# Kernel optimization log

Measured on AMD Instinct MI355X. Metric: run time of the kernel, lower is better.

The kernel has to match this reference:

```python
import jax, jax.numpy as jnp
import numpy as np

N_EMBED = 1024
N_HEADS = 16
HEAD_DIM = N_EMBED // N_HEADS


def setup_inputs() -> dict:
    key = jax.random.key(0)
    ks = jax.random.split(key, 5)
    x = jax.random.normal(ks[0], (4, 2048, N_EMBED), dtype=jnp.float32)
    # Linear params stored as [in, out] (y = x @ W + b), math-equivalent to torch Linear
    scale_attn = 1.0 / np.sqrt(N_EMBED)
    W_attn = jax.random.normal(ks[1], (N_EMBED, 3 * N_EMBED), dtype=jnp.float32) * scale_attn
    b_attn = jax.random.normal(ks[2], (3 * N_EMBED,), dtype=jnp.float32) * 0.02
    W_proj = jax.random.normal(ks[3], (N_EMBED, N_EMBED), dtype=jnp.float32) * scale_attn
    b_proj = jax.random.normal(ks[4], (N_EMBED,), dtype=jnp.float32) * 0.02
    return {"x": x, "W_attn": W_attn, "b_attn": b_attn, "W_proj": W_proj, "b_proj": b_proj}


def reference(x, W_attn, b_attn, W_proj, b_proj):
    BS, SL, ED = x.shape
    qkv = x @ W_attn + b_attn                      # [B, S, 3E]
    q, k, v = jnp.split(qkv, 3, axis=2)
    # [B, H, S, D]
    def heads(t):
        return t.reshape(BS, SL, N_HEADS, HEAD_DIM).transpose(0, 2, 1, 3)
    q, k, v = heads(q), heads(k), heads(v)
    att = jnp.einsum('bhqd,bhkd->bhqk', q, k) * (HEAD_DIM ** -0.5)
    causal = jnp.tril(jnp.ones((SL, SL), dtype=bool))
    att = jnp.where(causal[None, None], att, -jnp.inf)
    att = jax.nn.softmax(att, axis=-1)
    y = jnp.einsum('bhqk,bhkd->bhqd', att, v)      # [B, H, S, D]
    y = y.transpose(0, 2, 1, 3).reshape(BS, SL, ED)
    return y @ W_proj + b_proj
```

## Files before the change

kernel.cpp:

```cpp
#include <hip/hip_runtime.h>


#define BATCH 4
#define SEQ   2048
#define EMB   1024
#define NH    16
#define HD    64

typedef __bf16 bf16;
typedef __bf16 bf16x8 __attribute__((ext_vector_type(8)));
typedef float  f32x4  __attribute__((ext_vector_type(4)));

__device__ __forceinline__ void ld_lds16(const void* g, void* l) {
  __builtin_amdgcn_global_load_lds(
      (const __attribute__((address_space(1))) void*)g,
      (__attribute__((address_space(3))) void*)l, 16, 0, 0);
}

__global__ void cvt_f32_bf16(const float* __restrict__ in, bf16* __restrict__ out, int n) {
  int i = (blockIdx.x * blockDim.x + threadIdx.x) * 4;
  if (i + 3 < n) {
    float4 v = *(const float4*)(in + i);
    bf16 o0 = (bf16)v.x, o1 = (bf16)v.y, o2 = (bf16)v.z, o3 = (bf16)v.w;
    out[i] = o0; out[i+1] = o1; out[i+2] = o2; out[i+3] = o3;
  }
}

__global__ void transpose_cvt2(const float* __restrict__ Wa, const float* __restrict__ Wp,
                               bf16* __restrict__ WaT, bf16* __restrict__ WpT) {
  __shared__ float tile[32][33];
  int bx = blockIdx.x;
  const float* W; bf16* WT; int N;
  if (bx < 96) { W = Wa; WT = WaT; N = 3072; }
  else         { W = Wp; WT = WpT; N = 1024; bx -= 96; }
  int n0 = bx * 32, k0 = blockIdx.y * 32;
  int tx = threadIdx.x & 31, ty = threadIdx.x >> 5;
#pragma unroll
  for (int r = 0; r < 4; r++) {
    int k = k0 + ty + r * 8;
    tile[ty + r * 8][tx] = W[(long)k * N + n0 + tx];
  }
  __syncthreads();
#pragma unroll
  for (int r = 0; r < 4; r++) {
    int n = n0 + ty + r * 8;
    WT[(long)n * EMB + k0 + tx] = (bf16)tile[tx][ty + r * 8];
  }
}

#define QSCALE 0.18033688f

__global__ __launch_bounds__(256, 2) void gemm8p(
    const bf16* __restrict__ A, const bf16* __restrict__ Bt,
    const float* __restrict__ bias,
    bf16* __restrict__ q, bf16* __restrict__ k, bf16* __restrict__ v)
{
  __shared__ __align__(16) bf16 lds[24576];
  int lin = blockIdx.x;
  int xcd = lin & 7, s = lin >> 3;
  int by = xcd * 8 + (s & 7);
  int bx = s >> 3;
  int m0 = by * 128, n0 = bx * 256;
  int t = threadIdx.x;
  int wid = t >> 6, lane = t & 63;
  int l15 = lane & 15, quad = lane >> 4;
  int wc = wid;

  const bf16* Ag = A + (long)m0 * EMB;
  const bf16* Bg = Bt + (long)n0 * EMB;

  f32x4 acc[8][4] = {};
  bf16x8 af[8], bfr[4];
  constexpr int NT = EMB / 32;
  int ph8 = ((quad + (l15 >> 1)) & 3) * 8;

#define LDSA(b) (lds + (b) * 4096)
#define LDSB(b) (lds + 8192 + (b) * 8192)

#define ISSUE64(gbase, rowoff, ldst, ktt)                                      \
  { int r_ = (rowoff) + (t >> 2);                                              \
    int g_ = ((t & 3) - ((t >> 3) & 3)) & 3;                                   \
    ld_lds16(&(gbase)[(long)r_ * EMB + (ktt) + g_ * 8],                        \
             (ldst) + ((rowoff) + wid * 16) * 32); }

#define RD_A(mi) { int r_ = (mi) * 16 + l15;                                   \
    af[mi] = *(const bf16x8*)&Ab[r_ * 32 + ph8]; }
#define RD_B(ni) { int r_ = wc * 64 + (ni) * 16 + l15;                         \
    bfr[ni] = *(const bf16x8*)&Bb[r_ * 32 + ph8]; }

#define FENCE asm volatile("" ::: "memory")
#define BAR   { FENCE; __builtin_amdgcn_s_barrier(); FENCE; }

#define MFMAC(nlo)                                                             \
  { __builtin_amdgcn_s_setprio(1);                                             \
    _Pragma("unroll") for (int mi_ = 0; mi_ < 8; ++mi_)                        \
      _Pragma("unroll") for (int nj_ = 0; nj_ < 2; ++nj_)                      \
        acc[mi_][(nlo) + nj_] = __builtin_amdgcn_mfma_f32_16x16x32_bf16(       \
            af[mi_], bfr[(nlo) + nj_], acc[mi_][(nlo) + nj_], 0, 0, 0);        \
    __builtin_amdgcn_s_setprio(0); }

  ISSUE64(Ag, 0,   LDSA(0), 0);
  ISSUE64(Ag, 64,  LDSA(0), 0);
  ISSUE64(Bg, 0,   LDSB(0), 0);
  ISSUE64(Bg, 64,  LDSB(0), 0);
  ISSUE64(Bg, 128, LDSB(0), 0);
  ISSUE64(Bg, 192, LDSB(0), 0);
  ISSUE64(Ag, 0,   LDSA(1), 32);
  asm volatile("s_waitcnt vmcnt(1)" ::: "memory");
  BAR;

#pragma unroll 2
  for (int tt = 0; tt < NT; ++tt) {
    const bf16* Ab = LDSA(tt & 1);
    const bf16* Bb = LDSB(tt & 1);
    bf16* An = LDSA((tt + 1) & 1);
    bf16* Bn = LDSB((tt + 1) & 1);
    bf16* Ac = LDSA(tt & 1);
    int kn  = (tt + 1 < NT ? tt + 1 : NT - 1) * 32;
    int kn2 = (tt + 2 < NT ? tt + 2 : NT - 1) * 32;

#pragma unroll
    for (int mi = 0; mi < 8; ++mi) RD_A(mi);
    RD_B(0); RD_B(1);
    ISSUE64(Ag, 64,  An, kn);
    ISSUE64(Bg, 0,   Bn, kn);
    ISSUE64(Bg, 64,  Bn, kn);
    ISSUE64(Bg, 128, Bn, kn);
    BAR; MFMAC(0); BAR;
    RD_B(2); RD_B(3);
    ISSUE64(Bg, 192, Bn, kn);
    ISSUE64(Ag, 0,   Ac, kn2);
    asm volatile("s_waitcnt vmcnt(1)" ::: "memory");
    BAR; MFMAC(2); BAR;
  }

  asm volatile("s_waitcnt vmcnt(0)" ::: "memory");
  __syncthreads();

  int which = bx >> 2;
  if (which < 2) {
    bf16* dst = (which == 0) ? q : k;
    float scale = (which == 0) ? QSCALE : 1.0f;
#pragma unroll
    for (int mi = 0; mi < 8; ++mi)
#pragma unroll
      for (int ni = 0; ni < 4; ++ni) {
        int gcol = n0 + wc * 64 + ni * 16 + l15;
        float bv = bias[gcol];
        int e = gcol & 1023, h = e >> 6, d = e & 63;
#pragma unroll
        for (int i = 0; i < 4; ++i) {
          int grow = m0 + mi * 16 + quad * 4 + i;
          int b = grow >> 11, ss = grow & 2047;
          dst[(((long)b * NH + h) * SEQ + ss) * HD + d] =
              (bf16)((acc[mi][ni][i] + bv) * scale);
        }
      }
  } else {
#pragma unroll
    for (int mi = 0; mi < 8; ++mi)
#pragma unroll
      for (int ni = 0; ni < 4; ++ni) {
        int gcol = n0 + wc * 64 + ni * 16 + l15;
        float bv = bias[gcol];
        int e = gcol & 1023, h = e >> 6, d = e & 63;
#pragma unroll
        for (int i = 0; i < 4; ++i) {
          int grow = m0 + mi * 16 + quad * 4 + i;
          int b = grow >> 11, ss = grow & 2047;
          v[(((long)b * NH + h) * HD + d) * SEQ + ss] =
              (bf16)(acc[mi][ni][i] + bv);
        }
      }
  }
#undef LDSA
#undef LDSB
#undef ISSUE64
#undef RD_A
#undef RD_B
#undef MFMAC
}

__global__ __launch_bounds__(256, 3) void gemm_proj(
    const bf16* __restrict__ A, const bf16* __restrict__ Bt,
    const float* __restrict__ bias, float* __restrict__ out)
{
  __shared__ __align__(16) bf16 Al[128 * 64];
  __shared__ __align__(16) bf16 Bl[64 * 64];
  int lin = blockIdx.x;
  int xcd = lin & 7, s = lin >> 3;
  int bx = s >> 3, by = xcd * 8 + (s & 7);
  int m0 = by * 128;
  int n0 = bx * 64;
  int t = threadIdx.x;
  int wave = t >> 6, lane = t & 63;
  int l15 = lane & 15, quad = lane >> 4;
  int wm = (wave & 1) * 64, wn = (wave >> 1) * 32;

  f32x4 acc[4][2] = {};

  for (int kt = 0; kt < EMB; kt += 64) {
    __syncthreads();
#pragma unroll
    for (int it = 0; it < 4; ++it) {
      int c = it * 256 + t;
      int row = c >> 3, u = c & 7;
      ld_lds16(&A[(long)(m0 + row) * EMB + kt + ((u ^ (row & 7)) * 8)],
               &Al[(it * 256 + wave * 64) * 8]);
    }
    {
      int c = t;
      int row = c >> 3, u = c & 7;
      ld_lds16(&Bt[(long)(n0 + row) * EMB + kt + ((u ^ (row & 7)) * 8)],
               &Bl[(wave * 64) * 8]);
      c = 256 + t;
      row = c >> 3; u = c & 7;
      ld_lds16(&Bt[(long)(n0 + row) * EMB + kt + ((u ^ (row & 7)) * 8)],
               &Bl[(256 + wave * 64) * 8]);
    }
    __syncthreads();
#pragma unroll
    for (int ks = 0; ks < 2; ++ks) {
      bf16x8 af[4], bfr[2];
#pragma unroll
      for (int i = 0; i < 4; ++i) {
        int r = wm + i * 16 + l15;
        af[i] = *(const bf16x8*)(&Al[r * 64 + (((ks * 4 + quad) ^ (r & 7)) * 8)]);
      }
#pragma unroll
      for (int i = 0; i < 2; ++i) {
        int r = wn + i * 16 + l15;
        bfr[i] = *(const bf16x8*)(&Bl[r * 64 + (((ks * 4 + quad) ^ (r & 7)) * 8)]);
      }
#pragma unroll
      for (int mi = 0; mi < 4; ++mi)
#pragma unroll
        for (int ni = 0; ni < 2; ++ni)
          acc[mi][ni] = __builtin_amdgcn_mfma_f32_16x16x32_bf16(af[mi], bfr[ni], acc[mi][ni], 0, 0, 0);
    }
  }

#pragma unroll
  for (int mi = 0; mi < 4; ++mi)
#pragma unroll
    for (int ni = 0; ni < 2; ++ni) {
      int gcol = n0 + wn + ni * 16 + l15;
      float bv = bias[gcol];
#pragma unroll
      for (int i = 0; i < 4; ++i) {
        int grow = m0 + wm + mi * 16 + quad * 4 + i;
        out[(long)grow * EMB + gcol] = acc[mi][ni][i] + bv;
      }
    }
}

#define LDP 72

__global__ __launch_bounds__(256, 4) void attn(
    const bf16* __restrict__ Q, const bf16* __restrict__ K,
    const bf16* __restrict__ Vt, bf16* __restrict__ Y)
{
  __shared__ __align__(16) bf16 Kl[64 * 64];
  __shared__ __align__(16) bf16 Vl[64 * 64];
  __shared__ __align__(16) bf16 Pl[4][16 * LDP];
  int L = blockIdx.x;
  int a = L >> 3;
  int hd = (L & 7) + 8 * (a & 7);
  int pr = a >> 3;
  int b = hd >> 4, h = hd & 15;
  const bf16* Qp  = Q  + (((long)b * NH + h) * SEQ) * HD;
  const bf16* Kp  = K  + (((long)b * NH + h) * SEQ) * HD;
  const bf16* Vtp = Vt + (((long)b * NH + h) * HD) * SEQ;
  int t = threadIdx.x, wave = t >> 6, lane = t & 63;
  int l15 = lane & 15, quad = lane >> 4;

#pragma unroll 1
  for (int pass = 0; pass < 2; ++pass) {
    int sp = (pass == 0) ? (31 - pr) : pr;
    int q0 = sp * 64;
    int wq0 = q0 + wave * 16;

    bf16x8 qf[2];
    {
      const bf16* qrow = Qp + (long)(wq0 + l15) * HD + quad * 8;
      qf[0] = *(const bf16x8*)(qrow);
      qf[1] = *(const bf16x8*)(qrow + 32);
    }
    float lrow[4] = {};
    f32x4 oacc[4] = {};

    int ntiles = sp + 1;
#pragma unroll 1
    for (int kt = 0; kt < ntiles; ++kt) {
      int k0 = kt * 64;
      __syncthreads();
#pragma unroll
      for (int it = 0; it < 2; ++it) {
        int cu = it * 256 + t;
        int row = cu >> 3, u = cu & 7;
        ld_lds16(&Kp[(long)(k0 + row) * HD + ((u ^ (row & 7)) * 8)],
                 &Kl[(it * 256 + wave * 64) * 8]);
        ld_lds16(&Vtp[(long)row * SEQ + k0 + ((u ^ (row & 7)) * 8)],
                 &Vl[(it * 256 + wave * 64) * 8]);
      }
      __syncthreads();

      f32x4 sc[4] = {};
#pragma unroll
      for (int kk = 0; kk < 2; ++kk) {
#pragma unroll
        for (int ni = 0; ni < 4; ++ni) {
          int r = ni * 16 + l15, u = kk * 4 + quad;
          bf16x8 kfr = *(const bf16x8*)(&Kl[r * 64 + ((u ^ (r & 7)) * 8)]);
          sc[ni] = __builtin_amdgcn_mfma_f32_16x16x32_bf16(qf[kk], kfr, sc[ni], 0, 0, 0);
        }
      }

      bool full = (k0 + 63 <= wq0);
#pragma unroll
      for (int i = 0; i < 4; ++i) {
        int qr = wq0 + quad * 4 + i;
        float e[4];
#pragma unroll
        for (int ni = 0; ni < 4; ++ni) {
          float x = sc[ni][i];
          if (!full) x = (k0 + ni * 16 + l15 <= qr) ? x : -1e30f;
          e[ni] = __builtin_amdgcn_exp2f(x);
        }
        lrow[i] += (e[0] + e[1]) + (e[2] + e[3]);
        int prow = (quad * 4 + i) * LDP;
#pragma unroll
        for (int ni = 0; ni < 4; ++ni)
          Pl[wave][prow + ni * 16 + l15] = (bf16)e[ni];
      }
      asm volatile("s_waitcnt lgkmcnt(0)" ::: "memory");
#pragma unroll
      for (int kk = 0; kk < 2; ++kk) {
        int kbase = kk * 32 + quad * 8;
        bf16x8 pf = *(const bf16x8*)(&Pl[wave][(l15) * LDP + kbase]);
#pragma unroll
        for (int ni = 0; ni < 4; ++ni) {
          int dd = ni * 16 + l15, u = kk * 4 + quad;
          bf16x8 vf = *(const bf16x8*)(&Vl[dd * 64 + ((u ^ (dd & 7)) * 8)]);
          oacc[ni] = __builtin_amdgcn_mfma_f32_16x16x32_bf16(pf, vf, oacc[ni], 0, 0, 0);
        }
      }
    }
#pragma unroll
    for (int i = 0; i < 4; ++i) {
      float rs = lrow[i];
#pragma unroll
      for (int off = 8; off; off >>= 1) rs += __shfl_xor(rs, off, 16);
      float inv = 1.0f / rs;
      int qr = wq0 + quad * 4 + i;
      bf16* dst = Y + ((long)(b * SEQ + qr)) * EMB + h * HD;
#pragma unroll
      for (int ni = 0; ni < 4; ++ni)
        dst[ni * 16 + l15] = (bf16)(oacc[ni][i] * inv);
    }
  }
}

extern "C" void kernel_launch(void* const* d_in, const int* in_sizes, int n_in,
                              void* d_out, int out_size, void* d_ws, size_t ws_size,
                              hipStream_t stream) {
  const float* x      = (const float*)d_in[0];
  const float* W_attn = (const float*)d_in[1];
  const float* b_attn = (const float*)d_in[2];
  const float* W_proj = (const float*)d_in[3];
  const float* b_proj = (const float*)d_in[4];
  float* out = (float*)d_out;
  char* ws = (char*)d_ws;
  bf16* xb  = (bf16*)(ws);
  bf16* WaT = (bf16*)(ws + 16777216);
  bf16* WpT = (bf16*)(ws + 23068672);
  bf16* Qb  = (bf16*)(ws + 25165824);
  bf16* Kb  = (bf16*)(ws + 41943040);
  bf16* Vtb = (bf16*)(ws + 58720256);
  bf16* Yb  = (bf16*)(ws + 75497472);

  cvt_f32_bf16<<<8192, 256, 0, stream>>>(x, xb, BATCH * SEQ * EMB);
  transpose_cvt2<<<dim3(128, 32), 256, 0, stream>>>(W_attn, W_proj, WaT, WpT);
  gemm8p<<<768, 256, 0, stream>>>(xb, WaT, b_attn, Qb, Kb, Vtb);
  attn<<<1024, 256, 0, stream>>>(Qb, Kb, Vtb, Yb);
  gemm_proj<<<1024, 256, 0, stream>>>(Yb, WpT, b_proj, out);
}
```

Measured before the change: 248.2 us.

## Widen QKV GEMM tiles to 128x384 with 8 waves per block

The QKV projection GEMM now uses 512-thread blocks (8 waves), each computing a 128x384 output tile with 48 columns per wave, and launches 512 blocks instead of 768. Each k-step loads the A tile with a single 128-row issue, and the B tile grows to 384 rows in a larger LDS buffer. The aim is more reuse of each A tile per block and a grid that fits the CU count in one wave. The XCD-aware block swizzle is dropped for a plain row-major order, and the epilogue now decides Q/K/V per column because a tile can cross the Q/K/V boundaries. This may hurt L2 locality across XCDs and raises per-block LDS use.

After: 262.3 us. 5.7% more time.

```diff
diff --git a/kernel.cpp b/kernel.cpp
--- a/kernel.cpp
+++ b/kernel.cpp
@@ -50,17 +50,16 @@
 
 #define QSCALE 0.18033688f
 
-__global__ __launch_bounds__(256, 2) void gemm8p(
+__global__ __launch_bounds__(512, 2) void gemm_qkv(
     const bf16* __restrict__ A, const bf16* __restrict__ Bt,
     const float* __restrict__ bias,
     bf16* __restrict__ q, bf16* __restrict__ k, bf16* __restrict__ v)
 {
-  __shared__ __align__(16) bf16 lds[24576];
+  __shared__ __align__(16) bf16 lds[32768];
   int lin = blockIdx.x;
-  int xcd = lin & 7, s = lin >> 3;
-  int by = xcd * 8 + (s & 7);
-  int bx = s >> 3;
-  int m0 = by * 128, n0 = bx * 256;
+  int bx = lin & 7;
+  int by = lin >> 3;
+  int m0 = by * 128, n0 = bx * 384;
   int t = threadIdx.x;
   int wid = t >> 6, lane = t & 63;
   int l15 = lane & 15, quad = lane >> 4;
@@ -69,15 +68,15 @@
   const bf16* Ag = A + (long)m0 * EMB;
   const bf16* Bg = Bt + (long)n0 * EMB;
 
-  f32x4 acc[8][4] = {};
-  bf16x8 af[8], bfr[4];
+  f32x4 acc[8][3] = {};
+  bf16x8 af[8], bfr[3];
   constexpr int NT = EMB / 32;
   int ph8 = ((quad + (l15 >> 1)) & 3) * 8;
 
 #define LDSA(b) (lds + (b) * 4096)
-#define LDSB(b) (lds + 8192 + (b) * 8192)
-
-#define ISSUE64(gbase, rowoff, ldst, ktt)                                      \
+#define LDSB(b) (lds + 8192 + (b) * 12288)
+
+#define ISSUE128(gbase, rowoff, ldst, ktt)                                     \
   { int r_ = (rowoff) + (t >> 2);                                              \
     int g_ = ((t & 3) - ((t >> 3) & 3)) & 3;                                   \
     ld_lds16(&(gbase)[(long)r_ * EMB + (ktt) + g_ * 8],                        \
@@ -85,27 +84,34 @@
 
 #define RD_A(mi) { int r_ = (mi) * 16 + l15;                                   \
     af[mi] = *(const bf16x8*)&Ab[r_ * 32 + ph8]; }
-#define RD_B(ni) { int r_ = wc * 64 + (ni) * 16 + l15;                         \
+#define RD_B(ni) { int r_ = wc * 48 + (ni) * 16 + l15;                         \
     bfr[ni] = *(const bf16x8*)&Bb[r_ * 32 + ph8]; }
 
 #define FENCE asm volatile("" ::: "memory")
 #define BAR   { FENCE; __builtin_amdgcn_s_barrier(); FENCE; }
 
-#define MFMAC(nlo)                                                             \
+#define MFMAC2(n0_, n1_)                                                       \
+  { __builtin_amdgcn_s_setprio(1);                                             \
+    _Pragma("unroll") for (int mi_ = 0; mi_ < 8; ++mi_) {                      \
+      acc[mi_][n0_] = __builtin_amdgcn_mfma_f32_16x16x32_bf16(                 \
+          af[mi_], bfr[n0_], acc[mi_][n0_], 0, 0, 0);                          \
+      acc[mi_][n1_] = __builtin_amdgcn_mfma_f32_16x16x32_bf16(                 \
+          af[mi_], bfr[n1_], acc[mi_][n1_], 0, 0, 0);                          \
+    }                                                                          \
+    __builtin_amdgcn_s_setprio(0); }
+
+#define MFMAC1(n0_)                                                            \
   { __builtin_amdgcn_s_setprio(1);                                             \
     _Pragma("unroll") for (int mi_ = 0; mi_ < 8; ++mi_)                        \
-      _Pragma("unroll") for (int nj_ = 0; nj_ < 2; ++nj_)                      \
-        acc[mi_][(nlo) + nj_] = __builtin_amdgcn_mfma_f32_16x16x32_bf16(       \
-            af[mi_], bfr[(nlo) + nj_], acc[mi_][(nlo) + nj_], 0, 0, 0);        \
+      acc[mi_][n0_] = __builtin_amdgcn_mfma_f32_16x16x32_bf16(                 \
+          af[mi_], bfr[n0_], acc[mi_][n0_], 0, 0, 0);                          \
     __builtin_amdgcn_s_setprio(0); }
 
-  ISSUE64(Ag, 0,   LDSA(0), 0);
-  ISSUE64(Ag, 64,  LDSA(0), 0);
-  ISSUE64(Bg, 0,   LDSB(0), 0);
-  ISSUE64(Bg, 64,  LDSB(0), 0);
-  ISSUE64(Bg, 128, LDSB(0), 0);
-  ISSUE64(Bg, 192, LDSB(0), 0);
-  ISSUE64(Ag, 0,   LDSA(1), 32);
+  ISSUE128(Ag, 0,   LDSA(0), 0);
+  ISSUE128(Bg, 0,   LDSB(0), 0);
+  ISSUE128(Bg, 128, LDSB(0), 0);
+  ISSUE128(Bg, 256, LDSB(0), 0);
+  ISSUE128(Ag, 0,   LDSA(1), 32);
   asm volatile("s_waitcnt vmcnt(1)" ::: "memory");
   BAR;
 
@@ -113,7 +119,6 @@
   for (int tt = 0; tt < NT; ++tt) {
     const bf16* Ab = LDSA(tt & 1);
     const bf16* Bb = LDSB(tt & 1);
-    bf16* An = LDSA((tt + 1) & 1);
     bf16* Bn = LDSB((tt + 1) & 1);
     bf16* Ac = LDSA(tt & 1);
     int kn  = (tt + 1 < NT ? tt + 1 : NT - 1) * 32;
@@ -122,32 +127,30 @@
 #pragma unroll
     for (int mi = 0; mi < 8; ++mi) RD_A(mi);
     RD_B(0); RD_B(1);
-    ISSUE64(Ag, 64,  An, kn);
-    ISSUE64(Bg, 0,   Bn, kn);
-    ISSUE64(Bg, 64,  Bn, kn);
-    ISSUE64(Bg, 128, Bn, kn);
-    BAR; MFMAC(0); BAR;
-    RD_B(2); RD_B(3);
-    ISSUE64(Bg, 192, Bn, kn);
-    ISSUE64(Ag, 0,   Ac, kn2);
+    ISSUE128(Bg, 0,   Bn, kn);
+    ISSUE128(Bg, 128, Bn, kn);
+    BAR; MFMAC2(0, 1); BAR;
+    RD_B(2);
+    ISSUE128(Bg, 256, Bn, kn);
+    ISSUE128(Ag, 0,   Ac, kn2);
     asm volatile("s_waitcnt vmcnt(1)" ::: "memory");
-    BAR; MFMAC(2); BAR;
+    BAR; MFMAC1(2); BAR;
   }
 
   asm volatile("s_waitcnt vmcnt(0)" ::: "memory");
   __syncthreads();
 
-  int which = bx >> 2;
-  if (which < 2) {
-    bf16* dst = (which == 0) ? q : k;
-    float scale = (which == 0) ? QSCALE : 1.0f;
-#pragma unroll
-    for (int mi = 0; mi < 8; ++mi)
-#pragma unroll
-      for (int ni = 0; ni < 4; ++ni) {
-        int gcol = n0 + wc * 64 + ni * 16 + l15;
-        float bv = bias[gcol];
-        int e = gcol & 1023, h = e >> 6, d = e & 63;
+#pragma unroll
+  for (int mi = 0; mi < 8; ++mi)
+#pragma unroll
+    for (int ni = 0; ni < 3; ++ni) {
+      int gcol = n0 + wc * 48 + ni * 16 + l15;
+      float bv = bias[gcol];
+      int which = gcol >> 10;
+      int e = gcol & 1023, h = e >> 6, d = e & 63;
+      if (which < 2) {
+        bf16* dst = (which == 0) ? q : k;
+        float scale = (which == 0) ? QSCALE : 1.0f;
 #pragma unroll
         for (int i = 0; i < 4; ++i) {
           int grow = m0 + mi * 16 + quad * 4 + i;
@@ -155,15 +158,7 @@
           dst[(((long)b * NH + h) * SEQ + ss) * HD + d] =
               (bf16)((acc[mi][ni][i] + bv) * scale);
         }
-      }
-  } else {
-#pragma unroll
-    for (int mi = 0; mi < 8; ++mi)
-#pragma unroll
-      for (int ni = 0; ni < 4; ++ni) {
-        int gcol = n0 + wc * 64 + ni * 16 + l15;
-        float bv = bias[gcol];
-        int e = gcol & 1023, h = e >> 6, d = e & 63;
+      } else {
 #pragma unroll
         for (int i = 0; i < 4; ++i) {
           int grow = m0 + mi * 16 + quad * 4 + i;
@@ -172,13 +167,14 @@
               (bf16)(acc[mi][ni][i] + bv);
         }
       }
-  }
+    }
 #undef LDSA
 #undef LDSB
-#undef ISSUE64
+#undef ISSUE128
 #undef RD_A
 #undef RD_B
-#undef MFMAC
+#undef MFMAC2
+#undef MFMAC1
 }
 
 __global__ __launch_bounds__(256, 3) void gemm_proj(
@@ -381,7 +377,7 @@
 
   cvt_f32_bf16<<<8192, 256, 0, stream>>>(x, xb, BATCH * SEQ * EMB);
   transpose_cvt2<<<dim3(128, 32), 256, 0, stream>>>(W_attn, W_proj, WaT, WpT);
-  gemm8p<<<768, 256, 0, stream>>>(xb, WaT, b_attn, Qb, Kb, Vtb);
+  gemm_qkv<<<512, 512, 0, stream>>>(xb, WaT, b_attn, Qb, Kb, Vtb);
   attn<<<1024, 256, 0, stream>>>(Qb, Kb, Vtb, Yb);
   gemm_proj<<<1024, 256, 0, stream>>>(Yb, WpT, b_proj, out);
 }
```
